# Performance work log

Measured on AMD Instinct MI355X. Metric: run time of the kernel, lower is better.

The kernel has to match this reference:

```python
import jax, jax.numpy as jnp
import numpy as np

NX, NY = 512, 512
NT = 240
STRIDE = 4
H = 1e-3
DT = 5e-8
F0 = 100000.0
T0 = 6e-6
AMP = 1.0
GAUSS_A = 5e6
RHO = 1600.0
C_INIT = dict(C11=1e11, C22=1e10, C12=8e9, C16=2.5e10, C26=3e9, C66=1.2e10)
C_LO, C_HI = 1e9, 1e13


def setup_inputs() -> dict:
    # Ricker wavelet source signal (full time resolution)
    t = np.arange(NT) * DT
    tau = t - T0
    pf = (np.pi * F0 * tau) ** 2
    signal = (AMP * (1.0 - 2.0 * pf) * np.exp(-pf)).astype(np.float32)
    # Gaussian point-load spatial distribution centered at (0,0)
    Lx, Ly = H * (NX - 1), H * (NY - 1)
    x = np.linspace(-Lx / 2, Lx / 2, NX, dtype=np.float64)
    y = np.linspace(-Ly / 2, Ly / 2, NY, dtype=np.float64)
    X, Y = np.meshgrid(x, y, indexing='ij')
    r2 = X ** 2 + Y ** 2
    gauss = (GAUSS_A / np.pi * np.exp(-GAUSS_A * r2)).astype(np.float32)
    return {
        'log_C11': jnp.array([np.log(C_INIT['C11'])], dtype=jnp.float32),
        'log_C22': jnp.array([np.log(C_INIT['C22'])], dtype=jnp.float32),
        'log_C12': jnp.array([np.log(C_INIT['C12'])], dtype=jnp.float32),
        'log_C16': jnp.array([np.log(C_INIT['C16'])], dtype=jnp.float32),
        'log_C26': jnp.array([np.log(C_INIT['C26'])], dtype=jnp.float32),
        'log_C66': jnp.array([np.log(C_INIT['C66'])], dtype=jnp.float32),
        'rho': jnp.array([RHO], dtype=jnp.float32),
        'source_signal': jnp.asarray(signal),
        'gaussian_dist': jnp.asarray(gauss),
    }


def _stencils(u, h_inv_sq):
    # u: (B, nx, ny), zero-padded 3x3 FD stencils (conv2d_fixed equivalent)
    p = jnp.pad(u, ((0, 0), (1, 1), (1, 1)))
    dxx = (p[:, 2:, 1:-1] + p[:, :-2, 1:-1] - 2.0 * u) * h_inv_sq
    dyy = (p[:, 1:-1, 2:] + p[:, 1:-1, :-2] - 2.0 * u) * h_inv_sq
    dxy = 0.25 * (p[:, :-2, :-2] - p[:, :-2, 2:] - p[:, 2:, :-2] + p[:, 2:, 2:]) * h_inv_sq
    return dxx, dyy, dxy


def _simulate(log_Cs, rho, source_signal, gaussian_dist):
    log_C11, log_C22, log_C12, log_C16, log_C26, log_C66 = log_Cs
    C11 = jnp.clip(jnp.exp(log_C11[0]), C_LO, C_HI)
    C22 = jnp.clip(jnp.exp(log_C22[0]), C_LO, C_HI)
    C12 = jnp.clip(jnp.exp(log_C12[0]), C_LO, C_HI)
    C16 = jnp.clip(jnp.exp(log_C16[0]), C_LO, C_HI)
    C26 = jnp.clip(jnp.exp(log_C26[0]), C_LO, C_HI)
    C66 = jnp.clip(jnp.exp(log_C66[0]), C_LO, C_HI)
    r = rho[0]
    h_inv_sq = jnp.float32(1.0 / (H * H))
    dt2 = jnp.float32(DT * DT)
    g = gaussian_dist[None]  # (1, nx, ny)
    zeros = jnp.zeros((1, NX, NY), dtype=jnp.float32)

    def step(carry, f_amp):
        ux1, uy1, ux2, uy2 = carry
        # source on y component
        force_y = f_amp * g
        dxx_ux, dyy_ux, dxy_ux = _stencils(ux1, h_inv_sq)
        dxx_uy, dyy_uy, dxy_uy = _stencils(uy1, h_inv_sq)
        Lux = (C11 * dxx_ux + C66 * dyy_ux + (C12 + C66) * dxy_uy
               + 2.0 * C16 * dxy_ux + C16 * dxx_uy + C26 * dyy_uy) / r
        Luy = (C66 * dxx_uy + C22 * dyy_uy + (C12 + C66) * dxy_ux
               + C16 * dxx_ux + C26 * dyy_ux + 2.0 * C26 * dxy_uy + force_y) / r
        ux_new = 2.0 * ux1 - ux2 + dt2 * Lux
        uy_new = 2.0 * uy1 - uy2 + dt2 * Luy
        return (ux_new, uy_new, ux1, uy1), (ux_new, uy_new)

    init = (zeros, zeros, zeros, zeros)
    _, (ux_hist, uy_hist) = jax.lax.scan(step, init, source_signal)
    # (nt, 1, nx, ny) -> (1, nt, nx, ny), then PRIMARY time stride subsample
    ux_fields = jnp.moveaxis(ux_hist, 0, 1)[:, ::STRIDE]
    uy_fields = jnp.moveaxis(uy_hist, 0, 1)[:, ::STRIDE]
    return ux_fields, uy_fields


def reference(log_C11, log_C22, log_C12, log_C16, log_C26, log_C66, rho, source_signal, gaussian_dist):
    return _simulate((log_C11, log_C22, log_C12, log_C16, log_C26, log_C66),
                     rho, source_signal, gaussian_dist)
```

## Files before the change

kernel.cpp:

```cpp
#include <hip/hip_runtime.h>

#define NXg    512
#define Sg     262144
#define NFRg   60
#define Kg     8
#define NCHUNK 30
#define Tg     32
#define Eg     48
#define EJP    50
#define NSEGR  12
#define NTHR   576

__global__ __launch_bounds__(512)
void cfrp_init(float4* __restrict__ ws4)
{
    const int gt = (int)blockIdx.x * 512 + (int)threadIdx.x;
    ws4[gt] = make_float4(0.f, 0.f, 0.f, 0.f);
}

__global__ __launch_bounds__(NTHR)
void cfrp_chunk(const float* __restrict__ lc11, const float* __restrict__ lc22,
                const float* __restrict__ lc12, const float* __restrict__ lc16,
                const float* __restrict__ lc26, const float* __restrict__ lc66,
                const float* __restrict__ rho_p, const float* __restrict__ sig,
                const float* __restrict__ gauss, float* __restrict__ out,
                const float2* __restrict__ gcur, const float2* __restrict__ gprev,
                float2* __restrict__ ncur, float2* __restrict__ nprev,
                int TB)
{
    __shared__ float2 sf[2][Eg * EJP];

    const int tid = (int)threadIdx.x;
    const int w  = (int)blockIdx.x;
    const int q  = w & 7;
    const int r_ = w >> 3;
    const int ti = q * 2 + (r_ >> 4);
    const int tj = r_ & 15;
    const int oi = ti * Tg - Kg;
    const int oj = tj * Tg - Kg;

    const float C11 = fminf(fmaxf(expf(lc11[0]), 1e9f), 1e13f);
    const float C22 = fminf(fmaxf(expf(lc22[0]), 1e9f), 1e13f);
    const float C12 = fminf(fmaxf(expf(lc12[0]), 1e9f), 1e13f);
    const float C16 = fminf(fmaxf(expf(lc16[0]), 1e9f), 1e13f);
    const float C26 = fminf(fmaxf(expf(lc26[0]), 1e9f), 1e13f);
    const float C66 = fminf(fmaxf(expf(lc66[0]), 1e9f), 1e13f);
    const float rh   = rho_p[0];
    const float dt2  = 2.5e-15f;
    const float kk   = dt2 * 1e6f / rh;
    const float kc11 = kk * C11, kc22 = kk * C22, kc66 = kk * C66;
    const float kc16 = kk * C16, kc26 = kk * C26;
    const float kc1266 = kk * (C12 + C66);
    const float kc16x2 = 2.0f * kc16;
    const float kc26x2 = 2.0f * kc26;
    const float gsc = dt2 / rh;

    #pragma unroll
    for (int s = 0; s < 2; ++s) {
        const int p  = tid + s * NTHR;
        const int rr = p / 24;
        const int cp = (p - rr * 24) * 2;
        const int gi = oi + rr;
        const int gj = oj + cp;
        float4 v = make_float4(0.f, 0.f, 0.f, 0.f);
        if (((unsigned)gi < NXg) && ((unsigned)gj < NXg))
            v = *(const float4*)&gcur[gi * NXg + gj];
        const int li = rr * EJP + cp;
        *(float4*)&sf[0][li] = v;
        *(float4*)&sf[1][li] = v;
    }
    if (tid < Eg) {
        const int li = tid * EJP + Eg;
        *(float4*)&sf[0][li] = make_float4(0.f, 0.f, 0.f, 0.f);
        *(float4*)&sf[1][li] = make_float4(0.f, 0.f, 0.f, 0.f);
    }

    const int  srow = tid / NSEGR;
    const int  scol = tid - srow * NSEGR;
    const bool act  = (srow >= 1) && (srow <= Eg - 2);
    const int  c0   = scol * 4;
    const int  gi   = oi + srow;
    const int  gj0  = oj + c0;
    const int  idxC = srow * EJP + c0;
    const bool rin  = (unsigned)gi < NXg;
    bool inb0 = rin && ((unsigned)(gj0 + 0) < NXg);
    bool inb1 = rin && ((unsigned)(gj0 + 1) < NXg);
    bool inb2 = rin && ((unsigned)(gj0 + 2) < NXg);
    bool inb3 = rin && ((unsigned)(gj0 + 3) < NXg);
    const bool own = (srow >= Kg) && (srow < Kg + Tg) && (scol >= 2) && (scol <= 9);
    const int  go0 = gi * NXg + gj0;

    float2 pv0 = {0.f,0.f}, pv1 = {0.f,0.f}, pv2 = {0.f,0.f}, pv3 = {0.f,0.f};
    float  gf0 = 0.f, gf1 = 0.f, gf2 = 0.f, gf3 = 0.f;
    if (act && rin) {
        if ((unsigned)gj0 < NXg) {
            const float4 t = *(const float4*)&gprev[go0];
            pv0 = make_float2(t.x, t.y); pv1 = make_float2(t.z, t.w);
            const float4 g = *(const float4*)&gauss[go0];
            gf0 = g.x * gsc; gf1 = g.y * gsc; gf2 = g.z * gsc; gf3 = g.w * gsc;
        }
        if ((unsigned)(gj0 + 2) < NXg) {
            const float4 t = *(const float4*)&gprev[go0 + 2];
            pv2 = make_float2(t.x, t.y); pv3 = make_float2(t.z, t.w);
        }
    }
    __syncthreads();

    float2 cv0, cv1, cv2, cv3;
    {
        const float4 a = *(const float4*)&sf[0][idxC];
        const float4 b = *(const float4*)&sf[0][idxC + 2];
        cv0 = make_float2(a.x, a.y); cv1 = make_float2(a.z, a.w);
        cv2 = make_float2(b.x, b.y); cv3 = make_float2(b.z, b.w);
    }

    const float2* cur = sf[0];
    float2*       nxt = sf[1];

    #pragma unroll
    for (int st = 0; st < Kg; ++st) {
        const float fa = sig[TB + st];
        if (act) {
            const int iT = idxC - EJP;
            const int iB = idxC + EJP;
            const float4 t01 = *(const float4*)&cur[iT];
            const float4 t23 = *(const float4*)&cur[iT + 2];
            const float2 twv = cur[iT - 1];
            const float2 tev = cur[iT + 4];
            const float4 b01 = *(const float4*)&cur[iB];
            const float4 b23 = *(const float4*)&cur[iB + 2];
            const float2 bwv = cur[iB - 1];
            const float2 bev = cur[iB + 4];
            const float2 wmv = cur[idxC - 1];
            const float2 emv = cur[idxC + 4];

            const float2 ta0 = twv, ta1 = make_float2(t01.x, t01.y),
                         ta2 = make_float2(t01.z, t01.w),
                         ta3 = make_float2(t23.x, t23.y),
                         ta4 = make_float2(t23.z, t23.w), ta5 = tev;
            const float2 ba0 = bwv, ba1 = make_float2(b01.x, b01.y),
                         ba2 = make_float2(b01.z, b01.w),
                         ba3 = make_float2(b23.x, b23.y),
                         ba4 = make_float2(b23.z, b23.w), ba5 = bev;

            float2 nv0, nv1, nv2, nv3;
            #define CELLSTEP(nv, NW, N, NE, Wt, C, Et, SW, S, SE, P, GF, INB)   \
            {                                                                    \
                const float sxx_x = N.x + S.x - 2.0f * C.x;                      \
                const float syy_x = Wt.x + Et.x - 2.0f * C.x;                    \
                const float sxy_x = 0.25f * (NW.x - NE.x - SW.x + SE.x);         \
                const float sxx_y = N.y + S.y - 2.0f * C.y;                      \
                const float syy_y = Wt.y + Et.y - 2.0f * C.y;                    \
                const float sxy_y = 0.25f * (NW.y - NE.y - SW.y + SE.y);         \
                const float lux = kc11 * sxx_x + kc66 * syy_x + kc1266 * sxy_y   \
                                + kc16x2 * sxy_x + kc16 * sxx_y + kc26 * syy_y;  \
                const float luy = kc66 * sxx_y + kc22 * syy_y + kc1266 * sxy_x   \
                                + kc16 * sxx_x + kc26 * syy_x + kc26x2 * sxy_y   \
                                + fa * GF;                                       \
                float vx = 2.0f * C.x - P.x + lux;                               \
                float vy = 2.0f * C.y - P.y + luy;                               \
                vx = INB ? vx : 0.0f;                                            \
                vy = INB ? vy : 0.0f;                                            \
                nv = make_float2(vx, vy);                                        \
            }
            CELLSTEP(nv0, ta0, ta1, ta2, wmv, cv0, cv1, ba0, ba1, ba2, pv0, gf0, inb0)
            CELLSTEP(nv1, ta1, ta2, ta3, cv0, cv1, cv2, ba1, ba2, ba3, pv1, gf1, inb1)
            CELLSTEP(nv2, ta2, ta3, ta4, cv1, cv2, cv3, ba2, ba3, ba4, pv2, gf2, inb2)
            CELLSTEP(nv3, ta3, ta4, ta5, cv2, cv3, emv, ba3, ba4, ba5, pv3, gf3, inb3)
            #undef CELLSTEP

            pv0 = cv0; pv1 = cv1; pv2 = cv2; pv3 = cv3;
            cv0 = nv0; cv1 = nv1; cv2 = nv2; cv3 = nv3;

            *(float4*)&nxt[idxC]     = make_float4(cv0.x, cv0.y, cv1.x, cv1.y);
            *(float4*)&nxt[idxC + 2] = make_float4(cv2.x, cv2.y, cv3.x, cv3.y);

            if (((st & 3) == 0) && own) {
                const int fr = (TB + st) >> 2;
                *(float4*)&out[fr * Sg + go0] =
                    make_float4(cv0.x, cv1.x, cv2.x, cv3.x);
                *(float4*)&out[(fr + NFRg) * Sg + go0] =
                    make_float4(cv0.y, cv1.y, cv2.y, cv3.y);
            }
        }
        __syncthreads();
        float2* tmp = (float2*)cur; cur = nxt; nxt = tmp;
    }

    if (own) {
        *(float4*)&ncur[go0]      = make_float4(cv0.x, cv0.y, cv1.x, cv1.y);
        *(float4*)&ncur[go0 + 2]  = make_float4(cv2.x, cv2.y, cv3.x, cv3.y);
        *(float4*)&nprev[go0]     = make_float4(pv0.x, pv0.y, pv1.x, pv1.y);
        *(float4*)&nprev[go0 + 2] = make_float4(pv2.x, pv2.y, pv3.x, pv3.y);
    }
}

extern "C" void kernel_launch(void* const* d_in, const int* in_sizes, int n_in,
                              void* d_out, int out_size, void* d_ws, size_t ws_size,
                              hipStream_t stream) {
    const float* lc11  = (const float*)d_in[0];
    const float* lc22  = (const float*)d_in[1];
    const float* lc12  = (const float*)d_in[2];
    const float* lc16  = (const float*)d_in[3];
    const float* lc26  = (const float*)d_in[4];
    const float* lc66  = (const float*)d_in[5];
    const float* rho_p = (const float*)d_in[6];
    const float* sig   = (const float*)d_in[7];
    const float* gauss = (const float*)d_in[8];
    float* out  = (float*)d_out;
    float2* ws2 = (float2*)d_ws;

    float2* Ac = ws2;           float2* Ap = ws2 + Sg;
    float2* Bc = ws2 + 2 * Sg;  float2* Bp = ws2 + 3 * Sg;

    hipLaunchKernelGGL(cfrp_init, dim3(512), dim3(512), 0, stream, (float4*)d_ws);

    for (int c = 0; c < NCHUNK; ++c) {
        float2 *rc, *rp, *wc, *wp;
        if (c & 1) { rc = Bc; rp = Bp; wc = Ac; wp = Ap; }
        else       { rc = Ac; rp = Ap; wc = Bc; wp = Bp; }
        hipLaunchKernelGGL(cfrp_chunk, dim3(256), dim3(NTHR), 0, stream,
                           lc11, lc22, lc12, lc16, lc26, lc66, rho_p, sig,
                           gauss, out, rc, rp, wc, wp, c * Kg);
    }
}
```

Baseline: 548.0 us.

## Replace per-chunk kernel launches with persistent cooperative kernel using neighbor flags

Fuses the 30 chunk launches into one cooperative persistent kernel. Each tile block waits on per-tile flags set by its 8 neighbours instead of relying on kernel boundaries. Each block keeps its own interior tile in registers and shared memory across chunks, so it reloads only the halo from global memory. This removes launch overhead and part of the global traffic, at the cost of spin-wait polling with atomics and a dependence on the workspace being large enough. If the workspace is too small, the code falls back to the old multi-launch path.

```diff
diff --git a/kernel.cpp b/kernel.cpp
--- a/kernel.cpp
+++ b/kernel.cpp
@@ -10,25 +10,51 @@
 #define EJP    50
 #define NSEGR  12
 #define NTHR   576
-
-__global__ __launch_bounds__(512)
-void cfrp_init(float4* __restrict__ ws4)
+#define FLAGPAD 16
+
+#define WS_NEEDED (4ull * Sg * 8ull + 256ull * FLAGPAD * 4ull)
+
+#define CELLSTEP(nv, NW, N, NE, Wt, C, Et, SW, S, SE, P, GF, INB)            \
+{                                                                            \
+    const float sxx_x = N.x + S.x - 2.0f * C.x;                              \
+    const float syy_x = Wt.x + Et.x - 2.0f * C.x;                            \
+    const float sxy_x = 0.25f * (NW.x - NE.x - SW.x + SE.x);                 \
+    const float sxx_y = N.y + S.y - 2.0f * C.y;                              \
+    const float syy_y = Wt.y + Et.y - 2.0f * C.y;                            \
+    const float sxy_y = 0.25f * (NW.y - NE.y - SW.y + SE.y);                 \
+    const float lux = kc11 * sxx_x + kc66 * syy_x + kc1266 * sxy_y           \
+                    + kc16x2 * sxy_x + kc16 * sxx_y + kc26 * syy_y;          \
+    const float luy = kc66 * sxx_y + kc22 * syy_y + kc1266 * sxy_x           \
+                    + kc16 * sxx_x + kc26 * syy_x + kc26x2 * sxy_y           \
+                    + fa * GF;                                               \
+    float vx = 2.0f * C.x - P.x + lux;                                       \
+    float vy = 2.0f * C.y - P.y + luy;                                       \
+    vx = INB ? vx : 0.0f;                                                    \
+    vy = INB ? vy : 0.0f;                                                    \
+    nv = make_float2(vx, vy);                                                \
+}
+
+__global__ __launch_bounds__(256)
+void cfrp_zero_flags(int* __restrict__ flags)
 {
-    const int gt = (int)blockIdx.x * 512 + (int)threadIdx.x;
-    ws4[gt] = make_float4(0.f, 0.f, 0.f, 0.f);
+    flags[(int)threadIdx.x * FLAGPAD] = 0;
 }
 
 __global__ __launch_bounds__(NTHR)
-void cfrp_chunk(const float* __restrict__ lc11, const float* __restrict__ lc22,
-                const float* __restrict__ lc12, const float* __restrict__ lc16,
-                const float* __restrict__ lc26, const float* __restrict__ lc66,
-                const float* __restrict__ rho_p, const float* __restrict__ sig,
-                const float* __restrict__ gauss, float* __restrict__ out,
-                const float2* __restrict__ gcur, const float2* __restrict__ gprev,
-                float2* __restrict__ ncur, float2* __restrict__ nprev,
-                int TB)
+void cfrp_persist(const float* __restrict__ lc11, const float* __restrict__ lc22,
+                  const float* __restrict__ lc12, const float* __restrict__ lc16,
+                  const float* __restrict__ lc26, const float* __restrict__ lc66,
+                  const float* __restrict__ rho_p, const float* __restrict__ sig,
+                  const float* __restrict__ gauss, float* __restrict__ out,
+                  float2* __restrict__ ws)
 {
     __shared__ float2 sf[2][Eg * EJP];
+
+    float2* Gc0 = ws;
+    float2* Gp0 = ws + Sg;
+    float2* Gc1 = ws + 2 * (size_t)Sg;
+    float2* Gp1 = ws + 3 * (size_t)Sg;
+    int*  flags = (int*)(ws + 4 * (size_t)Sg);
 
     const int tid = (int)threadIdx.x;
     const int w  = (int)blockIdx.x;
@@ -38,6 +64,7 @@
     const int tj = r_ & 15;
     const int oi = ti * Tg - Kg;
     const int oj = tj * Tg - Kg;
+    const int myfl = (ti * 16 + tj) * FLAGPAD;
 
     const float C11 = fminf(fmaxf(expf(lc11[0]), 1e9f), 1e13f);
     const float C22 = fminf(fmaxf(expf(lc22[0]), 1e9f), 1e13f);
@@ -55,6 +82,209 @@
     const float kc26x2 = 2.0f * kc26;
     const float gsc = dt2 / rh;
 
+    {
+        float2* sflat = &sf[0][0];
+        #pragma unroll 1
+        for (int k = tid; k < 2 * Eg * EJP; k += NTHR)
+            sflat[k] = make_float2(0.f, 0.f);
+    }
+
+    const int  srow = tid / NSEGR;
+    const int  scol = tid - srow * NSEGR;
+    const bool act  = (srow >= 1) && (srow <= Eg - 2);
+    const int  c0   = scol * 4;
+    const int  gi   = oi + srow;
+    const int  gj0  = oj + c0;
+    const int  idxC = srow * EJP + c0;
+    const bool rin  = (unsigned)gi < NXg;
+    const bool inb0 = rin && ((unsigned)(gj0 + 0) < NXg);
+    const bool inb1 = rin && ((unsigned)(gj0 + 1) < NXg);
+    const bool inb2 = rin && ((unsigned)(gj0 + 2) < NXg);
+    const bool inb3 = rin && ((unsigned)(gj0 + 3) < NXg);
+    const bool own  = (srow >= Kg) && (srow < Kg + Tg) && (scol >= 2) && (scol <= 9);
+    const int  go0  = gi * NXg + gj0;
+
+    float  gf0 = 0.f, gf1 = 0.f, gf2 = 0.f, gf3 = 0.f;
+    if (act && rin && ((unsigned)gj0 < NXg)) {
+        const float4 g = *(const float4*)&gauss[go0];
+        gf0 = g.x * gsc; gf1 = g.y * gsc; gf2 = g.z * gsc; gf3 = g.w * gsc;
+    }
+    float2 pv0 = {0.f,0.f}, pv1 = {0.f,0.f}, pv2 = {0.f,0.f}, pv3 = {0.f,0.f};
+    float2 cv0 = {0.f,0.f}, cv1 = {0.f,0.f}, cv2 = {0.f,0.f}, cv3 = {0.f,0.f};
+
+    __syncthreads();
+
+    #pragma unroll 1
+    for (int c = 0; c < NCHUNK; ++c) {
+        if (c > 0) {
+            if (tid < 8) {
+                const int k2 = (tid < 4) ? tid : (tid + 1);
+                const int dr = k2 / 3 - 1, dc = k2 - (k2 / 3) * 3 - 1;
+                const int nti = ti + dr, ntj = tj + dc;
+                if ((unsigned)nti < 16u && (unsigned)ntj < 16u) {
+                    int* fp = &flags[(nti * 16 + ntj) * FLAGPAD];
+                    while (atomicAdd(fp, 0) < c)
+                        __builtin_amdgcn_s_sleep(2);
+                }
+            }
+            __syncthreads();
+            if (tid == 0) __threadfence();
+            __syncthreads();
+
+            const float2* Gc = (c & 1) ? Gc1 : Gc0;
+            const float2* Gp = (c & 1) ? Gp1 : Gp0;
+
+            #pragma unroll
+            for (int s = 0; s < 2; ++s) {
+                const int p  = tid + s * NTHR;
+                const int rr = p / 24;
+                const int cp = (p - rr * 24) * 2;
+                const bool skip = (rr >= Kg) && (rr < Kg + Tg) &&
+                                  (cp >= Kg) && (cp < Kg + Tg);
+                if (!skip) {
+                    const int gi2 = oi + rr, gj2 = oj + cp;
+                    float4 v = make_float4(0.f, 0.f, 0.f, 0.f);
+                    if (((unsigned)gi2 < NXg) && ((unsigned)gj2 < NXg))
+                        v = *(const float4*)&Gc[gi2 * NXg + gj2];
+                    *(float4*)&sf[0][rr * EJP + cp] = v;
+                }
+            }
+            if (act && !own) {
+                pv0 = pv1 = pv2 = pv3 = make_float2(0.f, 0.f);
+                if (rin) {
+                    if ((unsigned)gj0 < NXg) {
+                        const float4 t = *(const float4*)&Gp[go0];
+                        pv0 = make_float2(t.x, t.y); pv1 = make_float2(t.z, t.w);
+                    }
+                    if ((unsigned)(gj0 + 2) < NXg) {
+                        const float4 t = *(const float4*)&Gp[go0 + 2];
+                        pv2 = make_float2(t.x, t.y); pv3 = make_float2(t.z, t.w);
+                    }
+                }
+            }
+            __syncthreads();
+            if (act && !own) {
+                const float4 a = *(const float4*)&sf[0][idxC];
+                const float4 b = *(const float4*)&sf[0][idxC + 2];
+                cv0 = make_float2(a.x, a.y); cv1 = make_float2(a.z, a.w);
+                cv2 = make_float2(b.x, b.y); cv3 = make_float2(b.z, b.w);
+            }
+        }
+
+        const float2* cur = sf[0];
+        float2*       nxt = sf[1];
+        #pragma unroll
+        for (int st = 0; st < Kg; ++st) {
+            const float fa = sig[c * Kg + st];
+            if (act) {
+                const int iT = idxC - EJP;
+                const int iB = idxC + EJP;
+                const float4 t01 = *(const float4*)&cur[iT];
+                const float4 t23 = *(const float4*)&cur[iT + 2];
+                const float2 twv = cur[iT - 1];
+                const float2 tev = cur[iT + 4];
+                const float4 b01 = *(const float4*)&cur[iB];
+                const float4 b23 = *(const float4*)&cur[iB + 2];
+                const float2 bwv = cur[iB - 1];
+                const float2 bev = cur[iB + 4];
+                const float2 wmv = cur[idxC - 1];
+                const float2 emv = cur[idxC + 4];
+
+                const float2 ta0 = twv, ta1 = make_float2(t01.x, t01.y),
+                             ta2 = make_float2(t01.z, t01.w),
+                             ta3 = make_float2(t23.x, t23.y),
+                             ta4 = make_float2(t23.z, t23.w), ta5 = tev;
+                const float2 ba0 = bwv, ba1 = make_float2(b01.x, b01.y),
+                             ba2 = make_float2(b01.z, b01.w),
+                             ba3 = make_float2(b23.x, b23.y),
+                             ba4 = make_float2(b23.z, b23.w), ba5 = bev;
+
+                float2 nv0, nv1, nv2, nv3;
+                CELLSTEP(nv0, ta0, ta1, ta2, wmv, cv0, cv1, ba0, ba1, ba2, pv0, gf0, inb0)
+                CELLSTEP(nv1, ta1, ta2, ta3, cv0, cv1, cv2, ba1, ba2, ba3, pv1, gf1, inb1)
+                CELLSTEP(nv2, ta2, ta3, ta4, cv1, cv2, cv3, ba2, ba3, ba4, pv2, gf2, inb2)
+                CELLSTEP(nv3, ta3, ta4, ta5, cv2, cv3, emv, ba3, ba4, ba5, pv3, gf3, inb3)
+
+                pv0 = cv0; pv1 = cv1; pv2 = cv2; pv3 = cv3;
+                cv0 = nv0; cv1 = nv1; cv2 = nv2; cv3 = nv3;
+
+                *(float4*)&nxt[idxC]     = make_float4(cv0.x, cv0.y, cv1.x, cv1.y);
+                *(float4*)&nxt[idxC + 2] = make_float4(cv2.x, cv2.y, cv3.x, cv3.y);
+
+                if (((st & 3) == 0) && own) {
+                    const int fr = (c * Kg + st) >> 2;
+                    *(float4*)&out[fr * Sg + go0] =
+                        make_float4(cv0.x, cv1.x, cv2.x, cv3.x);
+                    *(float4*)&out[(fr + NFRg) * Sg + go0] =
+                        make_float4(cv0.y, cv1.y, cv2.y, cv3.y);
+                }
+            }
+            __syncthreads();
+            float2* tmp = (float2*)cur; cur = nxt; nxt = tmp;
+        }
+
+        {
+            float2* Pc = ((c + 1) & 1) ? Gc1 : Gc0;
+            float2* Pp = ((c + 1) & 1) ? Gp1 : Gp0;
+            if (own) {
+                *(float4*)&Pc[go0]     = make_float4(cv0.x, cv0.y, cv1.x, cv1.y);
+                *(float4*)&Pc[go0 + 2] = make_float4(cv2.x, cv2.y, cv3.x, cv3.y);
+                *(float4*)&Pp[go0]     = make_float4(pv0.x, pv0.y, pv1.x, pv1.y);
+                *(float4*)&Pp[go0 + 2] = make_float4(pv2.x, pv2.y, pv3.x, pv3.y);
+            }
+            __syncthreads();
+            if (tid == 0) {
+                __threadfence();
+                atomicExch(&flags[myfl], c + 1);
+            }
+        }
+    }
+}
+
+__global__ __launch_bounds__(512)
+void cfrp_init(float4* __restrict__ ws4)
+{
+    const int gt = (int)blockIdx.x * 512 + (int)threadIdx.x;
+    ws4[gt] = make_float4(0.f, 0.f, 0.f, 0.f);
+}
+
+__global__ __launch_bounds__(NTHR)
+void cfrp_chunk(const float* __restrict__ lc11, const float* __restrict__ lc22,
+                const float* __restrict__ lc12, const float* __restrict__ lc16,
+                const float* __restrict__ lc26, const float* __restrict__ lc66,
+                const float* __restrict__ rho_p, const float* __restrict__ sig,
+                const float* __restrict__ gauss, float* __restrict__ out,
+                const float2* __restrict__ gcur, const float2* __restrict__ gprev,
+                float2* __restrict__ ncur, float2* __restrict__ nprev,
+                int TB)
+{
+    __shared__ float2 sf[2][Eg * EJP];
+
+    const int tid = (int)threadIdx.x;
+    const int w  = (int)blockIdx.x;
+    const int q  = w & 7;
+    const int r_ = w >> 3;
+    const int ti = q * 2 + (r_ >> 4);
+    const int tj = r_ & 15;
+    const int oi = ti * Tg - Kg;
+    const int oj = tj * Tg - Kg;
+
+    const float C11 = fminf(fmaxf(expf(lc11[0]), 1e9f), 1e13f);
+    const float C22 = fminf(fmaxf(expf(lc22[0]), 1e9f), 1e13f);
+    const float C12 = fminf(fmaxf(expf(lc12[0]), 1e9f), 1e13f);
+    const float C16 = fminf(fmaxf(expf(lc16[0]), 1e9f), 1e13f);
+    const float C26 = fminf(fmaxf(expf(lc26[0]), 1e9f), 1e13f);
+    const float C66 = fminf(fmaxf(expf(lc66[0]), 1e9f), 1e13f);
+    const float rh   = rho_p[0];
+    const float dt2  = 2.5e-15f;
+    const float kk   = dt2 * 1e6f / rh;
+    const float kc11 = kk * C11, kc22 = kk * C22, kc66 = kk * C66;
+    const float kc16 = kk * C16, kc26 = kk * C26;
+    const float kc1266 = kk * (C12 + C66);
+    const float kc16x2 = 2.0f * kc16;
+    const float kc26x2 = 2.0f * kc26;
+    const float gsc = dt2 / rh;
+
     #pragma unroll
     for (int s = 0; s < 2; ++s) {
         const int p  = tid + s * NTHR;
@@ -83,12 +313,12 @@
     const int  gj0  = oj + c0;
     const int  idxC = srow * EJP + c0;
     const bool rin  = (unsigned)gi < NXg;
-    bool inb0 = rin && ((unsigned)(gj0 + 0) < NXg);
-    bool inb1 = rin && ((unsigned)(gj0 + 1) < NXg);
-    bool inb2 = rin && ((unsigned)(gj0 + 2) < NXg);
-    bool inb3 = rin && ((unsigned)(gj0 + 3) < NXg);
-    const bool own = (srow >= Kg) && (srow < Kg + Tg) && (scol >= 2) && (scol <= 9);
-    const int  go0 = gi * NXg + gj0;
+    const bool inb0 = rin && ((unsigned)(gj0 + 0) < NXg);
+    const bool inb1 = rin && ((unsigned)(gj0 + 1) < NXg);
+    const bool inb2 = rin && ((unsigned)(gj0 + 2) < NXg);
+    const bool inb3 = rin && ((unsigned)(gj0 + 3) < NXg);
+    const bool own  = (srow >= Kg) && (srow < Kg + Tg) && (scol >= 2) && (scol <= 9);
+    const int  go0  = gi * NXg + gj0;
 
     float2 pv0 = {0.f,0.f}, pv1 = {0.f,0.f}, pv2 = {0.f,0.f}, pv3 = {0.f,0.f};
     float  gf0 = 0.f, gf1 = 0.f, gf2 = 0.f, gf3 = 0.f;
@@ -144,30 +374,10 @@
                          ba4 = make_float2(b23.z, b23.w), ba5 = bev;
 
             float2 nv0, nv1, nv2, nv3;
-            #define CELLSTEP(nv, NW, N, NE, Wt, C, Et, SW, S, SE, P, GF, INB)   \
-            {                                                                    \
-                const float sxx_x = N.x + S.x - 2.0f * C.x;                      \
-                const float syy_x = Wt.x + Et.x - 2.0f * C.x;                    \
-                const float sxy_x = 0.25f * (NW.x - NE.x - SW.x + SE.x);         \
-                const float sxx_y = N.y + S.y - 2.0f * C.y;                      \
-                const float syy_y = Wt.y + Et.y - 2.0f * C.y;                    \
-                const float sxy_y = 0.25f * (NW.y - NE.y - SW.y + SE.y);         \
-                const float lux = kc11 * sxx_x + kc66 * syy_x + kc1266 * sxy_y   \
-                                + kc16x2 * sxy_x + kc16 * sxx_y + kc26 * syy_y;  \
-                const float luy = kc66 * sxx_y + kc22 * syy_y + kc1266 * sxy_x   \
-                                + kc16 * sxx_x + kc26 * syy_x + kc26x2 * sxy_y   \
-                                + fa * GF;                                       \
-                float vx = 2.0f * C.x - P.x + lux;                               \
-                float vy = 2.0f * C.y - P.y + luy;                               \
-                vx = INB ? vx : 0.0f;                                            \
-                vy = INB ? vy : 0.0f;                                            \
-                nv = make_float2(vx, vy);                                        \
-            }
             CELLSTEP(nv0, ta0, ta1, ta2, wmv, cv0, cv1, ba0, ba1, ba2, pv0, gf0, inb0)
             CELLSTEP(nv1, ta1, ta2, ta3, cv0, cv1, cv2, ba1, ba2, ba3, pv1, gf1, inb1)
             CELLSTEP(nv2, ta2, ta3, ta4, cv1, cv2, cv3, ba2, ba3, ba4, pv2, gf2, inb2)
             CELLSTEP(nv3, ta3, ta4, ta5, cv2, cv3, emv, ba3, ba4, ba5, pv3, gf3, inb3)
-            #undef CELLSTEP
 
             pv0 = cv0; pv1 = cv1; pv2 = cv2; pv3 = cv3;
             cv0 = nv0; cv1 = nv1; cv2 = nv2; cv3 = nv3;
@@ -210,17 +420,28 @@
     float* out  = (float*)d_out;
     float2* ws2 = (float2*)d_ws;
 
-    float2* Ac = ws2;           float2* Ap = ws2 + Sg;
-    float2* Bc = ws2 + 2 * Sg;  float2* Bp = ws2 + 3 * Sg;
-
-    hipLaunchKernelGGL(cfrp_init, dim3(512), dim3(512), 0, stream, (float4*)d_ws);
-
-    for (int c = 0; c < NCHUNK; ++c) {
-        float2 *rc, *rp, *wc, *wp;
-        if (c & 1) { rc = Bc; rp = Bp; wc = Ac; wp = Ap; }
-        else       { rc = Ac; rp = Ap; wc = Bc; wp = Bp; }
-        hipLaunchKernelGGL(cfrp_chunk, dim3(256), dim3(NTHR), 0, stream,
-                           lc11, lc22, lc12, lc16, lc26, lc66, rho_p, sig,
-                           gauss, out, rc, rp, wc, wp, c * Kg);
-    }
-}
+    if (ws_size >= WS_NEEDED) {
+        int* flags = (int*)(ws2 + 4 * (size_t)Sg);
+        hipLaunchKernelGGL(cfrp_zero_flags, dim3(1), dim3(256), 0, stream, flags);
+
+        void* args[] = { (void*)&lc11, (void*)&lc22, (void*)&lc12, (void*)&lc16,
+                         (void*)&lc26, (void*)&lc66, (void*)&rho_p, (void*)&sig,
+                         (void*)&gauss, (void*)&out, (void*)&ws2 };
+        hipLaunchCooperativeKernel((const void*)cfrp_persist, dim3(256),
+                                   dim3(NTHR), args, 0, stream);
+    } else {
+        float2* Ac = ws2;           float2* Ap = ws2 + Sg;
+        float2* Bc = ws2 + 2 * Sg;  float2* Bp = ws2 + 3 * Sg;
+
+        hipLaunchKernelGGL(cfrp_init, dim3(512), dim3(512), 0, stream, (float4*)d_ws);
+
+        for (int c = 0; c < NCHUNK; ++c) {
+            float2 *rc, *rp, *wc, *wp;
+            if (c & 1) { rc = Bc; rp = Bp; wc = Ac; wp = Ap; }
+            else       { rc = Ac; rp = Ap; wc = Bc; wp = Bp; }
+            hipLaunchKernelGGL(cfrp_chunk, dim3(256), dim3(NTHR), 0, stream,
+                               lc11, lc22, lc12, lc16, lc26, lc66, rho_p, sig,
+                               gauss, out, rc, rp, wc, wp, c * Kg);
+        }
+    }
+}
```

Result: slower. 945.1 us (+72.5%).

## Split interleaved ux/uy state into separate planar arrays in LDS and global

Applied to the files above, without the earlier changes.

Stores the x and y displacement components as separate planes (SoA) in both shared memory and the workspace instead of interleaved float2 pairs. Stencil neighbours become float4 row loads plus scalar halo loads per component, and frame outputs are written directly as float4 without shuffling components. The aim is to cut LDS bank conflicts and register repacking. In exchange it issues more separate LDS and global load instructions and changes the boundary masking to whole 4-wide groups, which is only valid when the domain width is a multiple of four.

```diff
diff --git a/kernel.cpp b/kernel.cpp
--- a/kernel.cpp
+++ b/kernel.cpp
@@ -7,7 +7,8 @@
 #define NCHUNK 30
 #define Tg     32
 #define Eg     48
-#define EJP    50
+#define Pg     52
+#define PLANE  (Eg * Pg)
 #define NSEGR  12
 #define NTHR   576
 
@@ -16,6 +17,24 @@
 {
     const int gt = (int)blockIdx.x * 512 + (int)threadIdx.x;
     ws4[gt] = make_float4(0.f, 0.f, 0.f, 0.f);
+}
+
+#define CELL(NXO, NYO, nwx,nnx,nex,wtx,ctx,etx,swx,ssx,sex,                  \
+                       nwy,nny,ney,wty,cty,ety,swy,ssy,sey, PX,PY,GF)        \
+{                                                                            \
+    const float sxx_x = nnx + ssx - 2.0f * ctx;                              \
+    const float syy_x = wtx + etx - 2.0f * ctx;                              \
+    const float sxy_x = 0.25f * (nwx - nex - swx + sex);                     \
+    const float sxx_y = nny + ssy - 2.0f * cty;                              \
+    const float syy_y = wty + ety - 2.0f * cty;                              \
+    const float sxy_y = 0.25f * (nwy - ney - swy + sey);                     \
+    const float lux = kc11 * sxx_x + kc66 * syy_x + kc1266 * sxy_y           \
+                    + kc16x2 * sxy_x + kc16 * sxx_y + kc26 * syy_y;          \
+    const float luy = kc66 * sxx_y + kc22 * syy_y + kc1266 * sxy_x           \
+                    + kc16 * sxx_x + kc26 * syy_x + kc26x2 * sxy_y           \
+                    + fa * GF;                                               \
+    NXO = 2.0f * ctx - PX + lux;                                             \
+    NYO = 2.0f * cty - PY + luy;                                             \
 }
 
 __global__ __launch_bounds__(NTHR)
@@ -24,11 +43,13 @@
                 const float* __restrict__ lc26, const float* __restrict__ lc66,
                 const float* __restrict__ rho_p, const float* __restrict__ sig,
                 const float* __restrict__ gauss, float* __restrict__ out,
-                const float2* __restrict__ gcur, const float2* __restrict__ gprev,
-                float2* __restrict__ ncur, float2* __restrict__ nprev,
+                const float* __restrict__ gcx, const float* __restrict__ gcy,
+                const float* __restrict__ gpx, const float* __restrict__ gpy,
+                float* __restrict__ ncx, float* __restrict__ ncy,
+                float* __restrict__ npx, float* __restrict__ npy,
                 int TB)
 {
-    __shared__ float2 sf[2][Eg * EJP];
+    __shared__ float sls[2][2][PLANE];
 
     const int tid = (int)threadIdx.x;
     const int w  = (int)blockIdx.x;
@@ -57,22 +78,28 @@
 
     #pragma unroll
     for (int s = 0; s < 2; ++s) {
-        const int p  = tid + s * NTHR;
-        const int rr = p / 24;
-        const int cp = (p - rr * 24) * 2;
-        const int gi = oi + rr;
-        const int gj = oj + cp;
+        const int p    = tid + s * NTHR;
+        const int rr   = p / 24;
+        const int rem  = p - rr * 24;
+        const int comp = rem / 12;
+        const int qc   = rem - comp * 12;
+        const int col4 = qc * 4;
+        const int gi   = oi + rr;
+        const int gj   = oj + col4;
         float4 v = make_float4(0.f, 0.f, 0.f, 0.f);
-        if (((unsigned)gi < NXg) && ((unsigned)gj < NXg))
-            v = *(const float4*)&gcur[gi * NXg + gj];
-        const int li = rr * EJP + cp;
-        *(float4*)&sf[0][li] = v;
-        *(float4*)&sf[1][li] = v;
-    }
-    if (tid < Eg) {
-        const int li = tid * EJP + Eg;
-        *(float4*)&sf[0][li] = make_float4(0.f, 0.f, 0.f, 0.f);
-        *(float4*)&sf[1][li] = make_float4(0.f, 0.f, 0.f, 0.f);
+        if (((unsigned)gi < NXg) && (gj >= 0) && (gj <= (int)NXg - 4)) {
+            const float* src = comp ? gcy : gcx;
+            v = *(const float4*)&src[gi * NXg + gj];
+        }
+        const int d = rr * Pg + col4;
+        *(float4*)&sls[0][comp][d] = v;
+        *(float4*)&sls[1][comp][d] = v;
+    }
+    if (tid < 2 * Eg) {
+        const int rr = tid >> 1, comp = tid & 1;
+        const int d = rr * Pg + Eg;
+        *(float4*)&sls[0][comp][d] = make_float4(0.f, 0.f, 0.f, 0.f);
+        *(float4*)&sls[1][comp][d] = make_float4(0.f, 0.f, 0.f, 0.f);
     }
 
     const int  srow = tid / NSEGR;
@@ -81,117 +108,83 @@
     const int  c0   = scol * 4;
     const int  gi   = oi + srow;
     const int  gj0  = oj + c0;
-    const int  idxC = srow * EJP + c0;
-    const bool rin  = (unsigned)gi < NXg;
-    bool inb0 = rin && ((unsigned)(gj0 + 0) < NXg);
-    bool inb1 = rin && ((unsigned)(gj0 + 1) < NXg);
-    bool inb2 = rin && ((unsigned)(gj0 + 2) < NXg);
-    bool inb3 = rin && ((unsigned)(gj0 + 3) < NXg);
-    const bool own = (srow >= Kg) && (srow < Kg + Tg) && (scol >= 2) && (scol <= 9);
-    const int  go0 = gi * NXg + gj0;
-
-    float2 pv0 = {0.f,0.f}, pv1 = {0.f,0.f}, pv2 = {0.f,0.f}, pv3 = {0.f,0.f};
-    float  gf0 = 0.f, gf1 = 0.f, gf2 = 0.f, gf3 = 0.f;
-    if (act && rin) {
-        if ((unsigned)gj0 < NXg) {
-            const float4 t = *(const float4*)&gprev[go0];
-            pv0 = make_float2(t.x, t.y); pv1 = make_float2(t.z, t.w);
-            const float4 g = *(const float4*)&gauss[go0];
-            gf0 = g.x * gsc; gf1 = g.y * gsc; gf2 = g.z * gsc; gf3 = g.w * gsc;
-        }
-        if ((unsigned)(gj0 + 2) < NXg) {
-            const float4 t = *(const float4*)&gprev[go0 + 2];
-            pv2 = make_float2(t.x, t.y); pv3 = make_float2(t.z, t.w);
-        }
+    const int  dC   = srow * Pg + c0;
+    const bool in4  = ((unsigned)gi < NXg) && (gj0 >= 0) && (gj0 <= (int)NXg - 4);
+    const bool own  = (srow >= Kg) && (srow < Kg + Tg) && (scol >= 2) && (scol <= 9);
+    const int  go0  = gi * NXg + gj0;
+
+    float4 pvx = {0,0,0,0}, pvy = {0,0,0,0}, gf4 = {0,0,0,0};
+    if (act && in4) {
+        pvx = *(const float4*)&gpx[go0];
+        pvy = *(const float4*)&gpy[go0];
+        const float4 g = *(const float4*)&gauss[go0];
+        gf4 = make_float4(g.x * gsc, g.y * gsc, g.z * gsc, g.w * gsc);
     }
     __syncthreads();
 
-    float2 cv0, cv1, cv2, cv3;
-    {
-        const float4 a = *(const float4*)&sf[0][idxC];
-        const float4 b = *(const float4*)&sf[0][idxC + 2];
-        cv0 = make_float2(a.x, a.y); cv1 = make_float2(a.z, a.w);
-        cv2 = make_float2(b.x, b.y); cv3 = make_float2(b.z, b.w);
-    }
-
-    const float2* cur = sf[0];
-    float2*       nxt = sf[1];
+    float4 cvx = *(const float4*)&sls[0][0][dC];
+    float4 cvy = *(const float4*)&sls[0][1][dC];
 
     #pragma unroll
     for (int st = 0; st < Kg; ++st) {
         const float fa = sig[TB + st];
+        const int cb = st & 1;
+        const float* sx = sls[cb][0];
+        const float* sy = sls[cb][1];
+        float* tx = sls[cb ^ 1][0];
+        float* ty = sls[cb ^ 1][1];
+
         if (act) {
-            const int iT = idxC - EJP;
-            const int iB = idxC + EJP;
-            const float4 t01 = *(const float4*)&cur[iT];
-            const float4 t23 = *(const float4*)&cur[iT + 2];
-            const float2 twv = cur[iT - 1];
-            const float2 tev = cur[iT + 4];
-            const float4 b01 = *(const float4*)&cur[iB];
-            const float4 b23 = *(const float4*)&cur[iB + 2];
-            const float2 bwv = cur[iB - 1];
-            const float2 bev = cur[iB + 4];
-            const float2 wmv = cur[idxC - 1];
-            const float2 emv = cur[idxC + 4];
-
-            const float2 ta0 = twv, ta1 = make_float2(t01.x, t01.y),
-                         ta2 = make_float2(t01.z, t01.w),
-                         ta3 = make_float2(t23.x, t23.y),
-                         ta4 = make_float2(t23.z, t23.w), ta5 = tev;
-            const float2 ba0 = bwv, ba1 = make_float2(b01.x, b01.y),
-                         ba2 = make_float2(b01.z, b01.w),
-                         ba3 = make_float2(b23.x, b23.y),
-                         ba4 = make_float2(b23.z, b23.w), ba5 = bev;
-
-            float2 nv0, nv1, nv2, nv3;
-            #define CELLSTEP(nv, NW, N, NE, Wt, C, Et, SW, S, SE, P, GF, INB)   \
-            {                                                                    \
-                const float sxx_x = N.x + S.x - 2.0f * C.x;                      \
-                const float syy_x = Wt.x + Et.x - 2.0f * C.x;                    \
-                const float sxy_x = 0.25f * (NW.x - NE.x - SW.x + SE.x);         \
-                const float sxx_y = N.y + S.y - 2.0f * C.y;                      \
-                const float syy_y = Wt.y + Et.y - 2.0f * C.y;                    \
-                const float sxy_y = 0.25f * (NW.y - NE.y - SW.y + SE.y);         \
-                const float lux = kc11 * sxx_x + kc66 * syy_x + kc1266 * sxy_y   \
-                                + kc16x2 * sxy_x + kc16 * sxx_y + kc26 * syy_y;  \
-                const float luy = kc66 * sxx_y + kc22 * syy_y + kc1266 * sxy_x   \
-                                + kc16 * sxx_x + kc26 * syy_x + kc26x2 * sxy_y   \
-                                + fa * GF;                                       \
-                float vx = 2.0f * C.x - P.x + lux;                               \
-                float vy = 2.0f * C.y - P.y + luy;                               \
-                vx = INB ? vx : 0.0f;                                            \
-                vy = INB ? vy : 0.0f;                                            \
-                nv = make_float2(vx, vy);                                        \
+            const int rN = dC - Pg, rS = dC + Pg;
+            const float4 Nx = *(const float4*)&sx[rN];
+            const float4 Sx = *(const float4*)&sx[rS];
+            const float  nwx = sx[rN - 1], nex = sx[rN + 4];
+            const float  swx = sx[rS - 1], sex = sx[rS + 4];
+            const float  wx  = sx[dC - 1], ex  = sx[dC + 4];
+            const float4 Ny = *(const float4*)&sy[rN];
+            const float4 Sy = *(const float4*)&sy[rS];
+            const float  nwy = sy[rN - 1], ney = sy[rN + 4];
+            const float  swy = sy[rS - 1], sey = sy[rS + 4];
+            const float  wy  = sy[dC - 1], ey  = sy[dC + 4];
+
+            float4 nx4, ny4;
+            CELL(nx4.x, ny4.x, nwx, Nx.x, Nx.y,  wx,   cvx.x, cvx.y, swx, Sx.x, Sx.y,
+                               nwy, Ny.x, Ny.y,  wy,   cvy.x, cvy.y, swy, Sy.x, Sy.y,
+                               pvx.x, pvy.x, gf4.x)
+            CELL(nx4.y, ny4.y, Nx.x, Nx.y, Nx.z, cvx.x, cvx.y, cvx.z, Sx.x, Sx.y, Sx.z,
+                               Ny.x, Ny.y, Ny.z, cvy.x, cvy.y, cvy.z, Sy.x, Sy.y, Sy.z,
+                               pvx.y, pvy.y, gf4.y)
+            CELL(nx4.z, ny4.z, Nx.y, Nx.z, Nx.w, cvx.y, cvx.z, cvx.w, Sx.y, Sx.z, Sx.w,
+                               Ny.y, Ny.z, Ny.w, cvy.y, cvy.z, cvy.w, Sy.y, Sy.z, Sy.w,
+                               pvx.z, pvy.z, gf4.z)
+            CELL(nx4.w, ny4.w, Nx.z, Nx.w, nex,  cvx.z, cvx.w, ex,    Sx.z, Sx.w, sex,
+                               Ny.z, Ny.w, ney,  cvy.z, cvy.w, ey,    Sy.z, Sy.w, sey,
+                               pvx.w, pvy.w, gf4.w)
+
+            if (!in4) {
+                nx4 = make_float4(0.f, 0.f, 0.f, 0.f);
+                ny4 = make_float4(0.f, 0.f, 0.f, 0.f);
             }
-            CELLSTEP(nv0, ta0, ta1, ta2, wmv, cv0, cv1, ba0, ba1, ba2, pv0, gf0, inb0)
-            CELLSTEP(nv1, ta1, ta2, ta3, cv0, cv1, cv2, ba1, ba2, ba3, pv1, gf1, inb1)
-            CELLSTEP(nv2, ta2, ta3, ta4, cv1, cv2, cv3, ba2, ba3, ba4, pv2, gf2, inb2)
-            CELLSTEP(nv3, ta3, ta4, ta5, cv2, cv3, emv, ba3, ba4, ba5, pv3, gf3, inb3)
-            #undef CELLSTEP
-
-            pv0 = cv0; pv1 = cv1; pv2 = cv2; pv3 = cv3;
-            cv0 = nv0; cv1 = nv1; cv2 = nv2; cv3 = nv3;
-
-            *(float4*)&nxt[idxC]     = make_float4(cv0.x, cv0.y, cv1.x, cv1.y);
-            *(float4*)&nxt[idxC + 2] = make_float4(cv2.x, cv2.y, cv3.x, cv3.y);
+            pvx = cvx; pvy = cvy;
+            cvx = nx4; cvy = ny4;
+
+            *(float4*)&tx[dC] = cvx;
+            *(float4*)&ty[dC] = cvy;
 
             if (((st & 3) == 0) && own) {
                 const int fr = (TB + st) >> 2;
-                *(float4*)&out[fr * Sg + go0] =
-                    make_float4(cv0.x, cv1.x, cv2.x, cv3.x);
-                *(float4*)&out[(fr + NFRg) * Sg + go0] =
-                    make_float4(cv0.y, cv1.y, cv2.y, cv3.y);
+                *(float4*)&out[fr * Sg + go0] = cvx;
+                *(float4*)&out[(fr + NFRg) * Sg + go0] = cvy;
             }
         }
         __syncthreads();
-        float2* tmp = (float2*)cur; cur = nxt; nxt = tmp;
     }
 
     if (own) {
-        *(float4*)&ncur[go0]      = make_float4(cv0.x, cv0.y, cv1.x, cv1.y);
-        *(float4*)&ncur[go0 + 2]  = make_float4(cv2.x, cv2.y, cv3.x, cv3.y);
-        *(float4*)&nprev[go0]     = make_float4(pv0.x, pv0.y, pv1.x, pv1.y);
-        *(float4*)&nprev[go0 + 2] = make_float4(pv2.x, pv2.y, pv3.x, pv3.y);
+        *(float4*)&ncx[go0] = cvx;
+        *(float4*)&ncy[go0] = cvy;
+        *(float4*)&npx[go0] = pvx;
+        *(float4*)&npy[go0] = pvy;
     }
 }
 
@@ -207,20 +200,29 @@
     const float* rho_p = (const float*)d_in[6];
     const float* sig   = (const float*)d_in[7];
     const float* gauss = (const float*)d_in[8];
-    float* out  = (float*)d_out;
-    float2* ws2 = (float2*)d_ws;
-
-    float2* Ac = ws2;           float2* Ap = ws2 + Sg;
-    float2* Bc = ws2 + 2 * Sg;  float2* Bp = ws2 + 3 * Sg;
+    float* out = (float*)d_out;
+    float* ws  = (float*)d_ws;
+
+    float* Acx = ws;          float* Acy = ws + Sg;
+    float* Apx = ws + 2 * Sg; float* Apy = ws + 3 * Sg;
+    float* Bcx = ws + 4 * Sg; float* Bcy = ws + 5 * Sg;
+    float* Bpx = ws + 6 * Sg; float* Bpy = ws + 7 * Sg;
 
     hipLaunchKernelGGL(cfrp_init, dim3(512), dim3(512), 0, stream, (float4*)d_ws);
 
     for (int c = 0; c < NCHUNK; ++c) {
-        float2 *rc, *rp, *wc, *wp;
-        if (c & 1) { rc = Bc; rp = Bp; wc = Ac; wp = Ap; }
-        else       { rc = Ac; rp = Ap; wc = Bc; wp = Bp; }
+        const float *rcx, *rcy, *rpx, *rpy;
+        float *wcx, *wcy, *wpx, *wpy;
+        if (c & 1) {
+            rcx = Bcx; rcy = Bcy; rpx = Bpx; rpy = Bpy;
+            wcx = Acx; wcy = Acy; wpx = Apx; wpy = Apy;
+        } else {
+            rcx = Acx; rcy = Acy; rpx = Apx; rpy = Apy;
+            wcx = Bcx; wcy = Bcy; wpx = Bpx; wpy = Bpy;
+        }
         hipLaunchKernelGGL(cfrp_chunk, dim3(256), dim3(NTHR), 0, stream,
                            lc11, lc22, lc12, lc16, lc26, lc66, rho_p, sig,
-                           gauss, out, rc, rp, wc, wp, c * Kg);
-    }
-}
+                           gauss, out, rcx, rcy, rpx, rpy,
+                           wcx, wcy, wpx, wpy, c * Kg);
+    }
+}
```

Result: slower. 580.9 us (+6.0%).

## Deepen temporal blocking to 12 steps per chunk with wider halo tile

Applied to the files above, without the earlier changes.

Raises the fused time steps per launch from 8 to 12 and enlarges the shared tile from 48 to 56 cells per side, so 20 chunk launches replace 30 and global read/write traffic per step drops. Threads are remapped to 16 per row (896 threads), leaving 2 of every 16 lanes idle, and the per-column bounds checks are collapsed into one per-4-cell predicate. The price is more redundant halo computation per tile (56x56 computed for 32x32 owned), a larger block, and more shared memory, which can lower occupancy.

```diff
diff --git a/kernel.cpp b/kernel.cpp
--- a/kernel.cpp
+++ b/kernel.cpp
@@ -3,19 +3,36 @@
 #define NXg    512
 #define Sg     262144
 #define NFRg   60
-#define Kg     8
-#define NCHUNK 30
+#define Kg     12
+#define NCHUNK 20
 #define Tg     32
-#define Eg     48
-#define EJP    50
-#define NSEGR  12
-#define NTHR   576
+#define Eg     56
+#define EJP    58
+#define NSEGR  14
+#define NTHR   896
+#define NPAIR  (Eg * (Eg / 2))
 
 __global__ __launch_bounds__(512)
 void cfrp_init(float4* __restrict__ ws4)
 {
     const int gt = (int)blockIdx.x * 512 + (int)threadIdx.x;
     ws4[gt] = make_float4(0.f, 0.f, 0.f, 0.f);
+}
+
+#define CELLSTEP(nv, NW, N, NE, Wt, C, Et, SW, S, SE, P, GF)                 \
+{                                                                            \
+    const float sxx_x = N.x + S.x - 2.0f * C.x;                              \
+    const float syy_x = Wt.x + Et.x - 2.0f * C.x;                            \
+    const float sxy_x = 0.25f * (NW.x - NE.x - SW.x + SE.x);                 \
+    const float sxx_y = N.y + S.y - 2.0f * C.y;                              \
+    const float syy_y = Wt.y + Et.y - 2.0f * C.y;                            \
+    const float sxy_y = 0.25f * (NW.y - NE.y - SW.y + SE.y);                 \
+    const float lux = kc11 * sxx_x + kc66 * syy_x + kc1266 * sxy_y           \
+                    + kc16x2 * sxy_x + kc16 * sxx_y + kc26 * syy_y;          \
+    const float luy = kc66 * sxx_y + kc22 * syy_y + kc1266 * sxy_x           \
+                    + kc16 * sxx_x + kc26 * syy_x + kc26x2 * sxy_y           \
+                    + fa * GF;                                               \
+    nv = make_float2(2.0f * C.x - P.x + lux, 2.0f * C.y - P.y + luy);        \
 }
 
 __global__ __launch_bounds__(NTHR)
@@ -57,59 +74,54 @@
 
     #pragma unroll
     for (int s = 0; s < 2; ++s) {
-        const int p  = tid + s * NTHR;
-        const int rr = p / 24;
-        const int cp = (p - rr * 24) * 2;
-        const int gi = oi + rr;
-        const int gj = oj + cp;
-        float4 v = make_float4(0.f, 0.f, 0.f, 0.f);
-        if (((unsigned)gi < NXg) && ((unsigned)gj < NXg))
-            v = *(const float4*)&gcur[gi * NXg + gj];
-        const int li = rr * EJP + cp;
-        *(float4*)&sf[0][li] = v;
-        *(float4*)&sf[1][li] = v;
+        const int p = tid + s * NTHR;
+        if (p < NPAIR) {
+            const int rr  = p / (Eg / 2);
+            const int cc2 = (p - rr * (Eg / 2)) * 2;
+            const int gi  = oi + rr;
+            const int gj  = oj + cc2;
+            float4 v = make_float4(0.f, 0.f, 0.f, 0.f);
+            if (((unsigned)gi < NXg) && ((unsigned)gj < NXg))
+                v = *(const float4*)&gcur[gi * NXg + gj];
+            const int d = rr * EJP + cc2;
+            *(float4*)&sf[0][d] = v;
+            *(float4*)&sf[1][d] = v;
+        }
     }
     if (tid < Eg) {
-        const int li = tid * EJP + Eg;
-        *(float4*)&sf[0][li] = make_float4(0.f, 0.f, 0.f, 0.f);
-        *(float4*)&sf[1][li] = make_float4(0.f, 0.f, 0.f, 0.f);
-    }
-
-    const int  srow = tid / NSEGR;
-    const int  scol = tid - srow * NSEGR;
-    const bool act  = (srow >= 1) && (srow <= Eg - 2);
+        const int d = tid * EJP + Eg;
+        *(float4*)&sf[0][d] = make_float4(0.f, 0.f, 0.f, 0.f);
+        *(float4*)&sf[1][d] = make_float4(0.f, 0.f, 0.f, 0.f);
+    }
+
+    const int  srow = tid >> 4;
+    const int  scol = tid & 15;
+    const bool act  = (scol < NSEGR) && (srow >= 1) && (srow <= Eg - 2);
     const int  c0   = scol * 4;
     const int  gi   = oi + srow;
     const int  gj0  = oj + c0;
-    const int  idxC = srow * EJP + c0;
-    const bool rin  = (unsigned)gi < NXg;
-    bool inb0 = rin && ((unsigned)(gj0 + 0) < NXg);
-    bool inb1 = rin && ((unsigned)(gj0 + 1) < NXg);
-    bool inb2 = rin && ((unsigned)(gj0 + 2) < NXg);
-    bool inb3 = rin && ((unsigned)(gj0 + 3) < NXg);
-    const bool own = (srow >= Kg) && (srow < Kg + Tg) && (scol >= 2) && (scol <= 9);
-    const int  go0 = gi * NXg + gj0;
-
-    float2 pv0 = {0.f,0.f}, pv1 = {0.f,0.f}, pv2 = {0.f,0.f}, pv3 = {0.f,0.f};
+    const int  dC   = srow * EJP + c0;
+    const bool in4  = ((unsigned)gi < NXg) && (gj0 >= 0) && (gj0 < (int)NXg);
+    const bool own  = act && (srow >= Kg) && (srow < Kg + Tg)
+                          && (scol >= 3) && (scol <= 10);
+    const int  go0  = gi * NXg + gj0;
+
+    float2 pv0 = {0,0}, pv1 = {0,0}, pv2 = {0,0}, pv3 = {0,0};
     float  gf0 = 0.f, gf1 = 0.f, gf2 = 0.f, gf3 = 0.f;
-    if (act && rin) {
-        if ((unsigned)gj0 < NXg) {
-            const float4 t = *(const float4*)&gprev[go0];
-            pv0 = make_float2(t.x, t.y); pv1 = make_float2(t.z, t.w);
-            const float4 g = *(const float4*)&gauss[go0];
-            gf0 = g.x * gsc; gf1 = g.y * gsc; gf2 = g.z * gsc; gf3 = g.w * gsc;
-        }
-        if ((unsigned)(gj0 + 2) < NXg) {
-            const float4 t = *(const float4*)&gprev[go0 + 2];
-            pv2 = make_float2(t.x, t.y); pv3 = make_float2(t.z, t.w);
-        }
+    if (act && in4) {
+        const float4 t0 = *(const float4*)&gprev[go0];
+        const float4 t1 = *(const float4*)&gprev[go0 + 2];
+        pv0 = make_float2(t0.x, t0.y); pv1 = make_float2(t0.z, t0.w);
+        pv2 = make_float2(t1.x, t1.y); pv3 = make_float2(t1.z, t1.w);
+        const float4 g = *(const float4*)&gauss[go0];
+        gf0 = g.x * gsc; gf1 = g.y * gsc; gf2 = g.z * gsc; gf3 = g.w * gsc;
     }
     __syncthreads();
 
     float2 cv0, cv1, cv2, cv3;
     {
-        const float4 a = *(const float4*)&sf[0][idxC];
-        const float4 b = *(const float4*)&sf[0][idxC + 2];
+        const float4 a = *(const float4*)&sf[0][dC];
+        const float4 b = *(const float4*)&sf[0][dC + 2];
         cv0 = make_float2(a.x, a.y); cv1 = make_float2(a.z, a.w);
         cv2 = make_float2(b.x, b.y); cv3 = make_float2(b.z, b.w);
     }
@@ -121,8 +133,8 @@
     for (int st = 0; st < Kg; ++st) {
         const float fa = sig[TB + st];
         if (act) {
-            const int iT = idxC - EJP;
-            const int iB = idxC + EJP;
+            const int iT = dC - EJP;
+            const int iB = dC + EJP;
             const float4 t01 = *(const float4*)&cur[iT];
             const float4 t23 = *(const float4*)&cur[iT + 2];
             const float2 twv = cur[iT - 1];
@@ -131,8 +143,8 @@
             const float4 b23 = *(const float4*)&cur[iB + 2];
             const float2 bwv = cur[iB - 1];
             const float2 bev = cur[iB + 4];
-            const float2 wmv = cur[idxC - 1];
-            const float2 emv = cur[idxC + 4];
+            const float2 wmv = cur[dC - 1];
+            const float2 emv = cur[dC + 4];
 
             const float2 ta0 = twv, ta1 = make_float2(t01.x, t01.y),
                          ta2 = make_float2(t01.z, t01.w),
@@ -144,36 +156,19 @@
                          ba4 = make_float2(b23.z, b23.w), ba5 = bev;
 
             float2 nv0, nv1, nv2, nv3;
-            #define CELLSTEP(nv, NW, N, NE, Wt, C, Et, SW, S, SE, P, GF, INB)   \
-            {                                                                    \
-                const float sxx_x = N.x + S.x - 2.0f * C.x;                      \
-                const float syy_x = Wt.x + Et.x - 2.0f * C.x;                    \
-                const float sxy_x = 0.25f * (NW.x - NE.x - SW.x + SE.x);         \
-                const float sxx_y = N.y + S.y - 2.0f * C.y;                      \
-                const float syy_y = Wt.y + Et.y - 2.0f * C.y;                    \
-                const float sxy_y = 0.25f * (NW.y - NE.y - SW.y + SE.y);         \
-                const float lux = kc11 * sxx_x + kc66 * syy_x + kc1266 * sxy_y   \
-                                + kc16x2 * sxy_x + kc16 * sxx_y + kc26 * syy_y;  \
-                const float luy = kc66 * sxx_y + kc22 * syy_y + kc1266 * sxy_x   \
-                                + kc16 * sxx_x + kc26 * syy_x + kc26x2 * sxy_y   \
-                                + fa * GF;                                       \
-                float vx = 2.0f * C.x - P.x + lux;                               \
-                float vy = 2.0f * C.y - P.y + luy;                               \
-                vx = INB ? vx : 0.0f;                                            \
-                vy = INB ? vy : 0.0f;                                            \
-                nv = make_float2(vx, vy);                                        \
+            CELLSTEP(nv0, ta0, ta1, ta2, wmv, cv0, cv1, ba0, ba1, ba2, pv0, gf0)
+            CELLSTEP(nv1, ta1, ta2, ta3, cv0, cv1, cv2, ba1, ba2, ba3, pv1, gf1)
+            CELLSTEP(nv2, ta2, ta3, ta4, cv1, cv2, cv3, ba2, ba3, ba4, pv2, gf2)
+            CELLSTEP(nv3, ta3, ta4, ta5, cv2, cv3, emv, ba3, ba4, ba5, pv3, gf3)
+
+            if (!in4) {
+                nv0 = nv1 = nv2 = nv3 = make_float2(0.f, 0.f);
             }
-            CELLSTEP(nv0, ta0, ta1, ta2, wmv, cv0, cv1, ba0, ba1, ba2, pv0, gf0, inb0)
-            CELLSTEP(nv1, ta1, ta2, ta3, cv0, cv1, cv2, ba1, ba2, ba3, pv1, gf1, inb1)
-            CELLSTEP(nv2, ta2, ta3, ta4, cv1, cv2, cv3, ba2, ba3, ba4, pv2, gf2, inb2)
-            CELLSTEP(nv3, ta3, ta4, ta5, cv2, cv3, emv, ba3, ba4, ba5, pv3, gf3, inb3)
-            #undef CELLSTEP
-
             pv0 = cv0; pv1 = cv1; pv2 = cv2; pv3 = cv3;
             cv0 = nv0; cv1 = nv1; cv2 = nv2; cv3 = nv3;
 
-            *(float4*)&nxt[idxC]     = make_float4(cv0.x, cv0.y, cv1.x, cv1.y);
-            *(float4*)&nxt[idxC + 2] = make_float4(cv2.x, cv2.y, cv3.x, cv3.y);
+            *(float4*)&nxt[dC]     = make_float4(cv0.x, cv0.y, cv1.x, cv1.y);
+            *(float4*)&nxt[dC + 2] = make_float4(cv2.x, cv2.y, cv3.x, cv3.y);
 
             if (((st & 3) == 0) && own) {
                 const int fr = (TB + st) >> 2;
```

After: 684.1 us. 1.25x slower.
